# Kernel tuning notes

Measured on AMD Instinct MI355X. Metric: run time of the kernel, lower is better.

## Reference

```python
import jax, jax.numpy as jnp
import numpy as np

B, N, D, K = 16, 1024, 512, 32
EPS = 1e-12  # F.normalize default eps


def setup_inputs() -> dict:
    key = jax.random.key(0)
    k1, k2, k3 = jax.random.split(key, 3)
    x = jax.random.normal(k1, (B, N, D), dtype=jnp.float32)
    mask = (jax.random.uniform(k2, (B, N)) < 0.9).astype(jnp.float32)
    centroids = jax.random.uniform(k3, (D, K), dtype=jnp.float32)
    # _init_params: conv.weight = 2*alpha*centroids, conv.bias = -alpha*||centroids||_col
    W = 2.0 * centroids
    b = -jnp.linalg.norm(centroids, axis=0)
    return {"x": x, "mask": mask, "W": W, "b": b, "centroids": centroids}


def reference(x, mask, W, b, centroids):
    # descriptor-wise L2 normalization (normalize_input=True)
    xn = x / jnp.maximum(jnp.linalg.norm(x, axis=2, keepdims=True), EPS)
    # 1x1 conv (matmul) + bias, masked logits
    logits = (jnp.einsum('bnd,dk->bnk', xn, W) + b) * mask[:, :, None]
    soft_assign = jax.nn.softmax(logits, axis=2) * mask[:, :, None]  # (B,N,K)
    # entropy with -log2(0) -> 0 (matches log_p[isinf]=0 since sa*0 = 0 there)
    safe = jnp.where(soft_assign > 0, soft_assign, 1.0)
    assign_entropy = -(soft_assign * jnp.log2(safe)).sum() / mask.sum()
    # cluster-usage distribution
    assign_sum = soft_assign.sum(axis=1)  # (B,K)
    assign_dist = jax.nn.log_softmax(assign_sum, axis=1)
    # NetVLAD residual pooling, algebraically fused (avoids (B,N,D,K) tensor):
    # vlad[b,d,k] = sum_n xn*sa - centroids[d,k]*sum_n sa
    vlad = jnp.einsum('bnd,bnk->bdk', xn, soft_assign) - centroids[None] * assign_sum[:, None, :]
    vlad = vlad / jnp.maximum(jnp.linalg.norm(vlad, axis=1, keepdims=True), EPS)
    vlad = jnp.transpose(vlad, (0, 2, 1))  # (B,K,D)
    return (vlad, assign_dist, assign_entropy)
```

## Files before the change

### kernel.cpp

```cpp
#include <hip/hip_runtime.h>
#include <math.h>

#define B 16
#define N 1024
#define D 512
#define K 32
#define EPSF 1e-12f

#define WS_WT_F   0
#define WS_CT_F   8192
#define WS_ASP_F  24576
#define WS_ENTP_F 57344
#define WS_MSKP_F 58368
#define WS_PART_F 59392

#define OFF_DIST 262144
#define OFF_ENT  262656

typedef __attribute__((ext_vector_type(8))) short s16x8;
typedef __attribute__((ext_vector_type(4))) short s16x4;
typedef __attribute__((ext_vector_type(4))) float f32x4;

__device__ __forceinline__ ushort f2b(float f) {
    unsigned u = __builtin_bit_cast(unsigned, f);
    u += 0x7fffu + ((u >> 16) & 1u);
    return (ushort)(u >> 16);
}
__device__ __forceinline__ float b2f(ushort u) {
    return __builtin_bit_cast(float, (unsigned)u << 16);
}

__global__ __launch_bounds__(256) void k0_prep(const float* __restrict__ Wf,
    const float* __restrict__ cent, float* __restrict__ ws)
{
    const int t = threadIdx.x;
    const int kk = t >> 3, dseg = (t & 7) * 64;
    if (blockIdx.x == 0) {
        ushort* wt = (ushort*)(ws + WS_WT_F);
        #pragma unroll
        for (int d8 = 0; d8 < 8; ++d8) {
            s16x8 v;
            #pragma unroll
            for (int e = 0; e < 8; ++e)
                v[e] = f2b(Wf[(dseg + d8 * 8 + e) * 32 + kk]);
            *(s16x8*)(wt + kk * 512 + dseg + d8 * 8) = v;
        }
    } else {
        float* ct = ws + WS_CT_F;
        #pragma unroll
        for (int d4 = 0; d4 < 16; ++d4) {
            float4 v;
            v.x = cent[(dseg + d4 * 4 + 0) * 32 + kk];
            v.y = cent[(dseg + d4 * 4 + 1) * 32 + kk];
            v.z = cent[(dseg + d4 * 4 + 2) * 32 + kk];
            v.w = cent[(dseg + d4 * 4 + 3) * 32 + kk];
            *(float4*)(ct + kk * 512 + dseg + d4 * 4) = v;
        }
    }
}

__global__ __launch_bounds__(256, 2) void kA(const float* __restrict__ x,
    const float* __restrict__ mask, const float* __restrict__ bias,
    float* __restrict__ ws, ushort* __restrict__ parts)
{
    __shared__ ushort xs[4 * 2048];
    __shared__ ushort xsT[512 * 36];
    __shared__ ushort tls[32 * 32];
    __shared__ float4 accsh[2 * 128];
    __shared__ float ssqsh[32], invsh[32];

    const int bid = blockIdx.x;
    const int b = bid >> 5;
    const int s = bid & 31;
    const int tid = threadIdx.x;
    const int w = tid >> 6;
    const int rw = w & 1, dw = w >> 1;
    const int l = tid & 63;
    const int g = l >> 4, lo = l & 15;
    const int n0 = s * 32 + rw * 16;
    const int p = bid * 2 + rw;
    const ushort* wt = (const ushort*)(ws + WS_WT_F);

    ushort* xw = xs + w * 2048;
    float ssq[8] = {0.f, 0.f, 0.f, 0.f, 0.f, 0.f, 0.f, 0.f};
    f32x4 acc[2] = {{0.f, 0.f, 0.f, 0.f}, {0.f, 0.f, 0.f, 0.f}};
    const float4* xg = (const float4*)(x + (size_t)(b * N + n0) * D);

    #pragma unroll
    for (int cc = 0; cc < 2; ++cc) {
        const int c = dw * 2 + cc;
        float4 fv[8];
        #pragma unroll
        for (int j = 0; j < 8; ++j) {
            int idx = l + 64 * j;
            fv[j] = xg[(idx >> 5) * 128 + c * 32 + (idx & 31)];
        }
        #pragma unroll
        for (int j = 0; j < 8; ++j)
            ssq[j] += fv[j].x * fv[j].x + fv[j].y * fv[j].y
                    + fv[j].z * fv[j].z + fv[j].w * fv[j].w;
        #pragma unroll
        for (int j = 0; j < 8; ++j) {
            int idx = l + 64 * j;
            int r = idx >> 5, c4 = idx & 31;
            unsigned bo = (unsigned)(c4 * 8) ^ (unsigned)((r & 7) << 4);
            s16x4 sv = { (short)f2b(fv[j].x), (short)f2b(fv[j].y),
                         (short)f2b(fv[j].z), (short)f2b(fv[j].w) };
            *(s16x4*)&xw[r * 128 + (bo >> 1)] = sv;
            int nn = rw * 16 + r;
            int dbase = c * 128 + c4 * 4;
            xsT[(dbase + 0) * 36 + nn] = (ushort)sv[0];
            xsT[(dbase + 1) * 36 + nn] = (ushort)sv[1];
            xsT[(dbase + 2) * 36 + nn] = (ushort)sv[2];
            xsT[(dbase + 3) * 36 + nn] = (ushort)sv[3];
        }
        #pragma unroll
        for (int ks = 0; ks < 4; ++ks) {
            unsigned bo = (unsigned)(ks * 64 + g * 16) ^ (unsigned)((lo & 7) << 4);
            s16x8 bfrag = *(const s16x8*)&xw[lo * 128 + (bo >> 1)];
            int dglob = c * 128 + ks * 32 + g * 8;
            s16x8 a0 = *(const s16x8*)(wt + (size_t)lo * 512 + dglob);
            s16x8 a1 = *(const s16x8*)(wt + (size_t)(16 + lo) * 512 + dglob);
            acc[0] = __builtin_amdgcn_mfma_f32_16x16x32_bf16(a0, bfrag, acc[0], 0, 0, 0);
            acc[1] = __builtin_amdgcn_mfma_f32_16x16x32_bf16(a1, bfrag, acc[1], 0, 0, 0);
        }
    }

    #pragma unroll
    for (int j = 0; j < 8; ++j) {
        #pragma unroll
        for (int m = 16; m; m >>= 1) ssq[j] += __shfl_xor(ssq[j], m);
    }
    if (dw == 1) {
        if ((l & 31) == 0) {
            #pragma unroll
            for (int j = 0; j < 8; ++j)
                ssqsh[rw * 16 + (l >> 5) + 2 * j] = ssq[j];
        }
        accsh[rw * 128 + l * 2 + 0] = *(float4*)&acc[0];
        accsh[rw * 128 + l * 2 + 1] = *(float4*)&acc[1];
    }
    __syncthreads();
    if (dw == 0) {
        float4 o0 = accsh[rw * 128 + l * 2 + 0];
        float4 o1 = accsh[rw * 128 + l * 2 + 1];
        acc[0][0] += o0.x; acc[0][1] += o0.y; acc[0][2] += o0.z; acc[0][3] += o0.w;
        acc[1][0] += o1.x; acc[1][1] += o1.y; acc[1][2] += o1.z; acc[1][3] += o1.w;
        if ((l & 31) == 0) {
            #pragma unroll
            for (int j = 0; j < 8; ++j) {
                int r = (l >> 5) + 2 * j;
                invsh[rw * 16 + r] = 1.f / fmaxf(sqrtf(ssq[j] + ssqsh[rw * 16 + r]), EPSF);
            }
        }
    }
    __syncthreads();
    if (dw == 0) {
        const float inv = invsh[rw * 16 + lo];
        const float mv = mask[b * N + n0 + lo];
        float lg[2][4];
        #pragma unroll
        for (int kt = 0; kt < 2; ++kt)
            #pragma unroll
            for (int r = 0; r < 4; ++r)
                lg[kt][r] = (acc[kt][r] * inv + bias[kt * 16 + g * 4 + r]) * mv;
        float mx = lg[0][0];
        #pragma unroll
        for (int kt = 0; kt < 2; ++kt)
            #pragma unroll
            for (int r = 0; r < 4; ++r) mx = fmaxf(mx, lg[kt][r]);
        mx = fmaxf(mx, __shfl_xor(mx, 16));
        mx = fmaxf(mx, __shfl_xor(mx, 32));
        float e[2][4], sum = 0.f;
        #pragma unroll
        for (int kt = 0; kt < 2; ++kt)
            #pragma unroll
            for (int r = 0; r < 4; ++r) { e[kt][r] = __expf(lg[kt][r] - mx); sum += e[kt][r]; }
        sum += __shfl_xor(sum, 16);
        sum += __shfl_xor(sum, 32);
        const float rs = mv / sum;
        float sa[2][4], ent = 0.f;
        #pragma unroll
        for (int kt = 0; kt < 2; ++kt)
            #pragma unroll
            for (int r = 0; r < 4; ++r) {
                sa[kt][r] = e[kt][r] * rs;
                ent += sa[kt][r] > 0.f ? -sa[kt][r] * __log2f(sa[kt][r]) : 0.f;
            }
        #pragma unroll
        for (int m = 32; m; m >>= 1) ent += __shfl_xor(ent, m);
        if (l == 0) ws[WS_ENTP_F + p] = ent;
        float mp = mv;
        #pragma unroll
        for (int m = 8; m; m >>= 1) mp += __shfl_xor(mp, m);
        if (l == 0) ws[WS_MSKP_F + p] = mp;
        #pragma unroll
        for (int kt = 0; kt < 2; ++kt)
            #pragma unroll
            for (int r = 0; r < 4; ++r) {
                float av = sa[kt][r];
                #pragma unroll
                for (int m = 8; m; m >>= 1) av += __shfl_xor(av, m);
                if (lo == 0) ws[WS_ASP_F + p * 32 + kt * 16 + g * 4 + r] = av;
            }
        #pragma unroll
        for (int kt = 0; kt < 2; ++kt)
            #pragma unroll
            for (int r = 0; r < 4; ++r)
                tls[(kt * 16 + g * 4 + r) * 32 + rw * 16 + lo] = f2b(sa[kt][r] * inv);
    }
    __syncthreads();

    f32x4 acc2[2][8];
    #pragma unroll
    for (int kt = 0; kt < 2; ++kt)
        #pragma unroll
        for (int dt = 0; dt < 8; ++dt)
            acc2[kt][dt] = (f32x4){0.f, 0.f, 0.f, 0.f};
    {
        s16x8 av0 = *(const s16x8*)&tls[lo * 32 + g * 8];
        s16x8 av1 = *(const s16x8*)&tls[(16 + lo) * 32 + g * 8];
        #pragma unroll
        for (int dt = 0; dt < 8; ++dt) {
            int d = w * 128 + dt * 16 + lo;
            s16x4 b0 = *(const s16x4*)&xsT[d * 36 + g * 8];
            s16x4 b1 = *(const s16x4*)&xsT[d * 36 + g * 8 + 4];
            s16x8 bv;
            bv[0] = b0[0]; bv[1] = b0[1]; bv[2] = b0[2]; bv[3] = b0[3];
            bv[4] = b1[0]; bv[5] = b1[1]; bv[6] = b1[2]; bv[7] = b1[3];
            acc2[0][dt] = __builtin_amdgcn_mfma_f32_16x16x32_bf16(av0, bv, acc2[0][dt], 0, 0, 0);
            acc2[1][dt] = __builtin_amdgcn_mfma_f32_16x16x32_bf16(av1, bv, acc2[1][dt], 0, 0, 0);
        }
    }
    __syncthreads();
    ushort* stg = xsT;
    #pragma unroll
    for (int kt = 0; kt < 2; ++kt)
        #pragma unroll
        for (int dt = 0; dt < 8; ++dt)
            #pragma unroll
            for (int r = 0; r < 4; ++r)
                stg[(kt * 16 + g * 4 + r) * 520 + w * 128 + dt * 16 + lo] = f2b(acc2[kt][dt][r]);
    __syncthreads();
    #pragma unroll
    for (int j = 0; j < 8; ++j) {
        int k = w * 8 + j;
        s16x8 v = *(const s16x8*)&stg[k * 520 + l * 8];
        *(s16x8*)(parts + ((size_t)(s * 16 + b) * 32 + k) * 512 + l * 8) = v;
    }
}

__global__ __launch_bounds__(128) void kC(const float* __restrict__ ws,
    const ushort* __restrict__ parts, float* __restrict__ out)
{
    __shared__ float pm[128];
    __shared__ float asL[32];
    __shared__ float red[2];
    const int bid = blockIdx.x;
    const int b = bid >> 5, k = bid & 31;
    const int t = threadIdx.x;
    {
        int kk = t & 31, i = t >> 5;
        float a = 0.f;
        #pragma unroll
        for (int ii = 0; ii < 16; ++ii)
            a += ws[WS_ASP_F + (size_t)(b * 64 + ii * 4 + i) * 32 + kk];
        pm[t] = a;
    }
    __syncthreads();
    if (t < 32) {
        float a = 0.f;
        #pragma unroll
        for (int i = 0; i < 4; ++i) a += pm[i * 32 + t];
        asL[t] = a;
    }
    __syncthreads();
    if (k == 0 && t < 32) {
        float a = asL[t];
        float mx = a;
        #pragma unroll
        for (int m = 16; m; m >>= 1) mx = fmaxf(mx, __shfl_xor(mx, m));
        float e = __expf(a - mx), ssum = e;
        #pragma unroll
        for (int m = 16; m; m >>= 1) ssum += __shfl_xor(ssum, m);
        out[OFF_DIST + b * 32 + t] = a - mx - logf(ssum);
    }
    if (bid == 0 && (t >> 6) == 1) {
        int l = t & 63;
        float es = 0.f, ms = 0.f;
        for (int i = l; i < 1024; i += 64) {
            es += ws[WS_ENTP_F + i];
            ms += ws[WS_MSKP_F + i];
        }
        #pragma unroll
        for (int m = 32; m; m >>= 1) { es += __shfl_xor(es, m); ms += __shfl_xor(ms, m); }
        if (l == 0) out[OFF_ENT] = es / ms;
    }
    const int d0 = t * 4;
    float a0 = 0.f, a1 = 0.f, a2 = 0.f, a3 = 0.f;
    for (int s = 0; s < 32; ++s) {
        s16x4 v = *(const s16x4*)(parts + ((size_t)(s * 16 + b) * 32 + k) * 512 + d0);
        a0 += b2f((ushort)v[0]);
        a1 += b2f((ushort)v[1]);
        a2 += b2f((ushort)v[2]);
        a3 += b2f((ushort)v[3]);
    }
    const float as = asL[k];
    float4 ct = *(const float4*)(ws + WS_CT_F + k * 512 + d0);
    float v0 = a0 - ct.x * as;
    float v1 = a1 - ct.y * as;
    float v2 = a2 - ct.z * as;
    float v3 = a3 - ct.w * as;
    float sq = v0 * v0 + v1 * v1 + v2 * v2 + v3 * v3;
    #pragma unroll
    for (int m = 32; m; m >>= 1) sq += __shfl_xor(sq, m);
    if ((t & 63) == 0) red[t >> 6] = sq;
    __syncthreads();
    float sc = 1.f / fmaxf(sqrtf(red[0] + red[1]), EPSF);
    float4 o = make_float4(v0 * sc, v1 * sc, v2 * sc, v3 * sc);
    *(float4*)(out + (size_t)(b * 32 + k) * 512 + d0) = o;
}

extern "C" void kernel_launch(void* const* d_in, const int* in_sizes, int n_in,
                              void* d_out, int out_size, void* d_ws, size_t ws_size,
                              hipStream_t stream)
{
    const float* x    = (const float*)d_in[0];
    const float* mask = (const float*)d_in[1];
    const float* W    = (const float*)d_in[2];
    const float* bias = (const float*)d_in[3];
    const float* cent = (const float*)d_in[4];
    float* out = (float*)d_out;
    float* ws  = (float*)d_ws;
    ushort* parts = (ushort*)(ws + WS_PART_F);

    k0_prep<<<dim3(2), dim3(256), 0, stream>>>(W, cent, ws);
    kA<<<dim3(512), dim3(256), 0, stream>>>(x, mask, bias, ws, parts);
    kC<<<dim3(512), dim3(128), 0, stream>>>(ws, parts, out);
}
```

Measured before the change: 36.04 us.

## Fuse weight prep into main kernel and process two token tiles per block

Removes the separate prep kernel. Each block of the main kernel now converts W to bf16 into a swizzled LDS buffer, keeps the A fragments in registers, and scatters the centroid transpose into the workspace. Each block handles 64 tokens in two tiles, so the grid drops to 256 blocks and the partial-sum buffer halves. The reduce kernel uses 256 threads and sums 16 partials instead of 32. The trade-off is that every block redoes the W conversion, register pressure rises, and fewer blocks are in flight.

```diff
diff --git a/kernel.cpp b/kernel.cpp
--- a/kernel.cpp
+++ b/kernel.cpp
@@ -7,12 +7,11 @@
 #define K 32
 #define EPSF 1e-12f
 
-#define WS_WT_F   0
-#define WS_CT_F   8192
-#define WS_ASP_F  24576
-#define WS_ENTP_F 57344
-#define WS_MSKP_F 58368
-#define WS_PART_F 59392
+#define WS_CT_F   0
+#define WS_ASP_F  16384
+#define WS_ENTP_F 49152
+#define WS_MSKP_F 50176
+#define WS_PART_F 51200
 
 #define OFF_DIST 262144
 #define OFF_ENT  262656
@@ -30,186 +29,68 @@
     return __builtin_bit_cast(float, (unsigned)u << 16);
 }
 
-__global__ __launch_bounds__(256) void k0_prep(const float* __restrict__ Wf,
-    const float* __restrict__ cent, float* __restrict__ ws)
-{
-    const int t = threadIdx.x;
-    const int kk = t >> 3, dseg = (t & 7) * 64;
-    if (blockIdx.x == 0) {
-        ushort* wt = (ushort*)(ws + WS_WT_F);
-        #pragma unroll
-        for (int d8 = 0; d8 < 8; ++d8) {
-            s16x8 v;
-            #pragma unroll
-            for (int e = 0; e < 8; ++e)
-                v[e] = f2b(Wf[(dseg + d8 * 8 + e) * 32 + kk]);
-            *(s16x8*)(wt + kk * 512 + dseg + d8 * 8) = v;
-        }
-    } else {
-        float* ct = ws + WS_CT_F;
-        #pragma unroll
-        for (int d4 = 0; d4 < 16; ++d4) {
-            float4 v;
-            v.x = cent[(dseg + d4 * 4 + 0) * 32 + kk];
-            v.y = cent[(dseg + d4 * 4 + 1) * 32 + kk];
-            v.z = cent[(dseg + d4 * 4 + 2) * 32 + kk];
-            v.w = cent[(dseg + d4 * 4 + 3) * 32 + kk];
-            *(float4*)(ct + kk * 512 + dseg + d4 * 4) = v;
-        }
-    }
-}
-
-__global__ __launch_bounds__(256, 2) void kA(const float* __restrict__ x,
-    const float* __restrict__ mask, const float* __restrict__ bias,
+struct SH {
+    union U {
+        ushort wtl[32 * 512];
+        struct Q {
+            ushort xs[4 * 2048];
+            ushort xsT[512 * 36];
+        } q;
+    } u;
+    ushort tls[32 * 32];
+    float4 accsh[2 * 128];
+    float ssqsh[32], invsh[32];
+};
+
+__global__ __launch_bounds__(256, 2) void kA2(const float* __restrict__ x,
+    const float* __restrict__ mask, const float* __restrict__ Wf,
+    const float* __restrict__ bias, const float* __restrict__ cent,
     float* __restrict__ ws, ushort* __restrict__ parts)
 {
-    __shared__ ushort xs[4 * 2048];
-    __shared__ ushort xsT[512 * 36];
-    __shared__ ushort tls[32 * 32];
-    __shared__ float4 accsh[2 * 128];
-    __shared__ float ssqsh[32], invsh[32];
-
+    __shared__ SH sh;
     const int bid = blockIdx.x;
-    const int b = bid >> 5;
-    const int s = bid & 31;
+    const int b = bid >> 4;
+    const int s64 = bid & 15;
     const int tid = threadIdx.x;
     const int w = tid >> 6;
     const int rw = w & 1, dw = w >> 1;
     const int l = tid & 63;
     const int g = l >> 4, lo = l & 15;
-    const int n0 = s * 32 + rw * 16;
-    const int p = bid * 2 + rw;
-    const ushort* wt = (const ushort*)(ws + WS_WT_F);
-
-    ushort* xw = xs + w * 2048;
-    float ssq[8] = {0.f, 0.f, 0.f, 0.f, 0.f, 0.f, 0.f, 0.f};
-    f32x4 acc[2] = {{0.f, 0.f, 0.f, 0.f}, {0.f, 0.f, 0.f, 0.f}};
-    const float4* xg = (const float4*)(x + (size_t)(b * N + n0) * D);
-
-    #pragma unroll
-    for (int cc = 0; cc < 2; ++cc) {
-        const int c = dw * 2 + cc;
-        float4 fv[8];
-        #pragma unroll
-        for (int j = 0; j < 8; ++j) {
-            int idx = l + 64 * j;
-            fv[j] = xg[(idx >> 5) * 128 + c * 32 + (idx & 31)];
-        }
-        #pragma unroll
-        for (int j = 0; j < 8; ++j)
-            ssq[j] += fv[j].x * fv[j].x + fv[j].y * fv[j].y
-                    + fv[j].z * fv[j].z + fv[j].w * fv[j].w;
-        #pragma unroll
-        for (int j = 0; j < 8; ++j) {
-            int idx = l + 64 * j;
-            int r = idx >> 5, c4 = idx & 31;
-            unsigned bo = (unsigned)(c4 * 8) ^ (unsigned)((r & 7) << 4);
-            s16x4 sv = { (short)f2b(fv[j].x), (short)f2b(fv[j].y),
-                         (short)f2b(fv[j].z), (short)f2b(fv[j].w) };
-            *(s16x4*)&xw[r * 128 + (bo >> 1)] = sv;
-            int nn = rw * 16 + r;
-            int dbase = c * 128 + c4 * 4;
-            xsT[(dbase + 0) * 36 + nn] = (ushort)sv[0];
-            xsT[(dbase + 1) * 36 + nn] = (ushort)sv[1];
-            xsT[(dbase + 2) * 36 + nn] = (ushort)sv[2];
-            xsT[(dbase + 3) * 36 + nn] = (ushort)sv[3];
-        }
+
+    if (tid < 64) {
+        int k = tid & 31, dd = tid >> 5;
+        int d = bid * 2 + dd;
+        ws[WS_CT_F + k * 512 + d] = cent[d * 32 + k];
+    }
+    {
+        const float4* Wg = (const float4*)Wf;
+        #pragma unroll
+        for (int i = 0; i < 16; ++i) {
+            int f4 = tid + i * 256;
+            float4 v = Wg[f4];
+            int d = f4 >> 3, k4 = (f4 & 7) << 2;
+            float vv[4] = {v.x, v.y, v.z, v.w};
+            #pragma unroll
+            for (int j = 0; j < 4; ++j) {
+                int k = k4 + j;
+                sh.u.wtl[(k * 512 + d) ^ ((k & 7) << 3)] = f2b(vv[j]);
+            }
+        }
+    }
+    __syncthreads();
+    s16x8 afr0[2][4], afr1[2][4];
+    #pragma unroll
+    for (int cc = 0; cc < 2; ++cc)
         #pragma unroll
         for (int ks = 0; ks < 4; ++ks) {
-            unsigned bo = (unsigned)(ks * 64 + g * 16) ^ (unsigned)((lo & 7) << 4);
-            s16x8 bfrag = *(const s16x8*)&xw[lo * 128 + (bo >> 1)];
-            int dglob = c * 128 + ks * 32 + g * 8;
-            s16x8 a0 = *(const s16x8*)(wt + (size_t)lo * 512 + dglob);
-            s16x8 a1 = *(const s16x8*)(wt + (size_t)(16 + lo) * 512 + dglob);
-            acc[0] = __builtin_amdgcn_mfma_f32_16x16x32_bf16(a0, bfrag, acc[0], 0, 0, 0);
-            acc[1] = __builtin_amdgcn_mfma_f32_16x16x32_bf16(a1, bfrag, acc[1], 0, 0, 0);
-        }
-    }
-
-    #pragma unroll
-    for (int j = 0; j < 8; ++j) {
-        #pragma unroll
-        for (int m = 16; m; m >>= 1) ssq[j] += __shfl_xor(ssq[j], m);
-    }
-    if (dw == 1) {
-        if ((l & 31) == 0) {
-            #pragma unroll
-            for (int j = 0; j < 8; ++j)
-                ssqsh[rw * 16 + (l >> 5) + 2 * j] = ssq[j];
-        }
-        accsh[rw * 128 + l * 2 + 0] = *(float4*)&acc[0];
-        accsh[rw * 128 + l * 2 + 1] = *(float4*)&acc[1];
-    }
-    __syncthreads();
-    if (dw == 0) {
-        float4 o0 = accsh[rw * 128 + l * 2 + 0];
-        float4 o1 = accsh[rw * 128 + l * 2 + 1];
-        acc[0][0] += o0.x; acc[0][1] += o0.y; acc[0][2] += o0.z; acc[0][3] += o0.w;
-        acc[1][0] += o1.x; acc[1][1] += o1.y; acc[1][2] += o1.z; acc[1][3] += o1.w;
-        if ((l & 31) == 0) {
-            #pragma unroll
-            for (int j = 0; j < 8; ++j) {
-                int r = (l >> 5) + 2 * j;
-                invsh[rw * 16 + r] = 1.f / fmaxf(sqrtf(ssq[j] + ssqsh[rw * 16 + r]), EPSF);
-            }
-        }
-    }
-    __syncthreads();
-    if (dw == 0) {
-        const float inv = invsh[rw * 16 + lo];
-        const float mv = mask[b * N + n0 + lo];
-        float lg[2][4];
-        #pragma unroll
-        for (int kt = 0; kt < 2; ++kt)
-            #pragma unroll
-            for (int r = 0; r < 4; ++r)
-                lg[kt][r] = (acc[kt][r] * inv + bias[kt * 16 + g * 4 + r]) * mv;
-        float mx = lg[0][0];
-        #pragma unroll
-        for (int kt = 0; kt < 2; ++kt)
-            #pragma unroll
-            for (int r = 0; r < 4; ++r) mx = fmaxf(mx, lg[kt][r]);
-        mx = fmaxf(mx, __shfl_xor(mx, 16));
-        mx = fmaxf(mx, __shfl_xor(mx, 32));
-        float e[2][4], sum = 0.f;
-        #pragma unroll
-        for (int kt = 0; kt < 2; ++kt)
-            #pragma unroll
-            for (int r = 0; r < 4; ++r) { e[kt][r] = __expf(lg[kt][r] - mx); sum += e[kt][r]; }
-        sum += __shfl_xor(sum, 16);
-        sum += __shfl_xor(sum, 32);
-        const float rs = mv / sum;
-        float sa[2][4], ent = 0.f;
-        #pragma unroll
-        for (int kt = 0; kt < 2; ++kt)
-            #pragma unroll
-            for (int r = 0; r < 4; ++r) {
-                sa[kt][r] = e[kt][r] * rs;
-                ent += sa[kt][r] > 0.f ? -sa[kt][r] * __log2f(sa[kt][r]) : 0.f;
-            }
-        #pragma unroll
-        for (int m = 32; m; m >>= 1) ent += __shfl_xor(ent, m);
-        if (l == 0) ws[WS_ENTP_F + p] = ent;
-        float mp = mv;
-        #pragma unroll
-        for (int m = 8; m; m >>= 1) mp += __shfl_xor(mp, m);
-        if (l == 0) ws[WS_MSKP_F + p] = mp;
-        #pragma unroll
-        for (int kt = 0; kt < 2; ++kt)
-            #pragma unroll
-            for (int r = 0; r < 4; ++r) {
-                float av = sa[kt][r];
-                #pragma unroll
-                for (int m = 8; m; m >>= 1) av += __shfl_xor(av, m);
-                if (lo == 0) ws[WS_ASP_F + p * 32 + kt * 16 + g * 4 + r] = av;
-            }
-        #pragma unroll
-        for (int kt = 0; kt < 2; ++kt)
-            #pragma unroll
-            for (int r = 0; r < 4; ++r)
-                tls[(kt * 16 + g * 4 + r) * 32 + rw * 16 + lo] = f2b(sa[kt][r] * inv);
-    }
-    __syncthreads();
+            int dglob = (dw * 2 + cc) * 128 + ks * 32 + g * 8;
+            afr0[cc][ks] = *(const s16x8*)&sh.u.wtl[(lo * 512 + dglob) ^ ((lo & 7) << 3)];
+            afr1[cc][ks] = *(const s16x8*)&sh.u.wtl[((16 + lo) * 512 + dglob) ^ ((lo & 7) << 3)];
+        }
+    __syncthreads();
+
+    ushort* xw = sh.u.q.xs + w * 2048;
+    ushort* xsT = sh.u.q.xsT;
 
     f32x4 acc2[2][8];
     #pragma unroll
@@ -217,23 +98,157 @@
         #pragma unroll
         for (int dt = 0; dt < 8; ++dt)
             acc2[kt][dt] = (f32x4){0.f, 0.f, 0.f, 0.f};
-    {
-        s16x8 av0 = *(const s16x8*)&tls[lo * 32 + g * 8];
-        s16x8 av1 = *(const s16x8*)&tls[(16 + lo) * 32 + g * 8];
-        #pragma unroll
-        for (int dt = 0; dt < 8; ++dt) {
-            int d = w * 128 + dt * 16 + lo;
-            s16x4 b0 = *(const s16x4*)&xsT[d * 36 + g * 8];
-            s16x4 b1 = *(const s16x4*)&xsT[d * 36 + g * 8 + 4];
-            s16x8 bv;
-            bv[0] = b0[0]; bv[1] = b0[1]; bv[2] = b0[2]; bv[3] = b0[3];
-            bv[4] = b1[0]; bv[5] = b1[1]; bv[6] = b1[2]; bv[7] = b1[3];
-            acc2[0][dt] = __builtin_amdgcn_mfma_f32_16x16x32_bf16(av0, bv, acc2[0][dt], 0, 0, 0);
-            acc2[1][dt] = __builtin_amdgcn_mfma_f32_16x16x32_bf16(av1, bv, acc2[1][dt], 0, 0, 0);
-        }
-    }
-    __syncthreads();
-    ushort* stg = xsT;
+
+    #pragma unroll
+    for (int tile = 0; tile < 2; ++tile) {
+        const int n0 = s64 * 64 + tile * 32 + rw * 16;
+        const int p = bid * 4 + tile * 2 + rw;
+
+        float ssq[8] = {0.f, 0.f, 0.f, 0.f, 0.f, 0.f, 0.f, 0.f};
+        f32x4 acc[2] = {{0.f, 0.f, 0.f, 0.f}, {0.f, 0.f, 0.f, 0.f}};
+        const float4* xg = (const float4*)(x + (size_t)(b * N + n0) * D);
+
+        #pragma unroll
+        for (int cc = 0; cc < 2; ++cc) {
+            const int c = dw * 2 + cc;
+            float4 fv[8];
+            #pragma unroll
+            for (int j = 0; j < 8; ++j) {
+                int idx = l + 64 * j;
+                fv[j] = xg[(idx >> 5) * 128 + c * 32 + (idx & 31)];
+            }
+            #pragma unroll
+            for (int j = 0; j < 8; ++j)
+                ssq[j] += fv[j].x * fv[j].x + fv[j].y * fv[j].y
+                        + fv[j].z * fv[j].z + fv[j].w * fv[j].w;
+            #pragma unroll
+            for (int j = 0; j < 8; ++j) {
+                int idx = l + 64 * j;
+                int r = idx >> 5, c4 = idx & 31;
+                unsigned bo = (unsigned)(c4 * 8) ^ (unsigned)((r & 7) << 4);
+                s16x4 sv = { (short)f2b(fv[j].x), (short)f2b(fv[j].y),
+                             (short)f2b(fv[j].z), (short)f2b(fv[j].w) };
+                *(s16x4*)&xw[r * 128 + (bo >> 1)] = sv;
+                int nn = rw * 16 + r;
+                int dbase = c * 128 + c4 * 4;
+                xsT[(dbase + 0) * 36 + nn] = (ushort)sv[0];
+                xsT[(dbase + 1) * 36 + nn] = (ushort)sv[1];
+                xsT[(dbase + 2) * 36 + nn] = (ushort)sv[2];
+                xsT[(dbase + 3) * 36 + nn] = (ushort)sv[3];
+            }
+            #pragma unroll
+            for (int ks = 0; ks < 4; ++ks) {
+                unsigned bo = (unsigned)(ks * 64 + g * 16) ^ (unsigned)((lo & 7) << 4);
+                s16x8 bfrag = *(const s16x8*)&xw[lo * 128 + (bo >> 1)];
+                acc[0] = __builtin_amdgcn_mfma_f32_16x16x32_bf16(afr0[cc][ks], bfrag, acc[0], 0, 0, 0);
+                acc[1] = __builtin_amdgcn_mfma_f32_16x16x32_bf16(afr1[cc][ks], bfrag, acc[1], 0, 0, 0);
+            }
+        }
+
+        #pragma unroll
+        for (int j = 0; j < 8; ++j) {
+            #pragma unroll
+            for (int m = 16; m; m >>= 1) ssq[j] += __shfl_xor(ssq[j], m);
+        }
+        if (dw == 1) {
+            if ((l & 31) == 0) {
+                #pragma unroll
+                for (int j = 0; j < 8; ++j)
+                    sh.ssqsh[rw * 16 + (l >> 5) + 2 * j] = ssq[j];
+            }
+            sh.accsh[rw * 128 + l * 2 + 0] = *(float4*)&acc[0];
+            sh.accsh[rw * 128 + l * 2 + 1] = *(float4*)&acc[1];
+        }
+        __syncthreads();
+        if (dw == 0) {
+            float4 o0 = sh.accsh[rw * 128 + l * 2 + 0];
+            float4 o1 = sh.accsh[rw * 128 + l * 2 + 1];
+            acc[0][0] += o0.x; acc[0][1] += o0.y; acc[0][2] += o0.z; acc[0][3] += o0.w;
+            acc[1][0] += o1.x; acc[1][1] += o1.y; acc[1][2] += o1.z; acc[1][3] += o1.w;
+            if ((l & 31) == 0) {
+                #pragma unroll
+                for (int j = 0; j < 8; ++j) {
+                    int r = (l >> 5) + 2 * j;
+                    sh.invsh[rw * 16 + r] = 1.f / fmaxf(sqrtf(ssq[j] + sh.ssqsh[rw * 16 + r]), EPSF);
+                }
+            }
+        }
+        __syncthreads();
+        if (dw == 0) {
+            const float inv = sh.invsh[rw * 16 + lo];
+            const float mv = mask[b * N + n0 + lo];
+            float lg[2][4];
+            #pragma unroll
+            for (int kt = 0; kt < 2; ++kt)
+                #pragma unroll
+                for (int r = 0; r < 4; ++r)
+                    lg[kt][r] = (acc[kt][r] * inv + bias[kt * 16 + g * 4 + r]) * mv;
+            float mx = lg[0][0];
+            #pragma unroll
+            for (int kt = 0; kt < 2; ++kt)
+                #pragma unroll
+                for (int r = 0; r < 4; ++r) mx = fmaxf(mx, lg[kt][r]);
+            mx = fmaxf(mx, __shfl_xor(mx, 16));
+            mx = fmaxf(mx, __shfl_xor(mx, 32));
+            float e[2][4], sum = 0.f;
+            #pragma unroll
+            for (int kt = 0; kt < 2; ++kt)
+                #pragma unroll
+                for (int r = 0; r < 4; ++r) { e[kt][r] = __expf(lg[kt][r] - mx); sum += e[kt][r]; }
+            sum += __shfl_xor(sum, 16);
+            sum += __shfl_xor(sum, 32);
+            const float rs = mv / sum;
+            float sa[2][4], ent = 0.f;
+            #pragma unroll
+            for (int kt = 0; kt < 2; ++kt)
+                #pragma unroll
+                for (int r = 0; r < 4; ++r) {
+                    sa[kt][r] = e[kt][r] * rs;
+                    ent += sa[kt][r] > 0.f ? -sa[kt][r] * __log2f(sa[kt][r]) : 0.f;
+                }
+            #pragma unroll
+            for (int m = 32; m; m >>= 1) ent += __shfl_xor(ent, m);
+            if (l == 0) ws[WS_ENTP_F + p] = ent;
+            float mp = mv;
+            #pragma unroll
+            for (int m = 8; m; m >>= 1) mp += __shfl_xor(mp, m);
+            if (l == 0) ws[WS_MSKP_F + p] = mp;
+            #pragma unroll
+            for (int kt = 0; kt < 2; ++kt)
+                #pragma unroll
+                for (int r = 0; r < 4; ++r) {
+                    float av = sa[kt][r];
+                    #pragma unroll
+                    for (int m = 8; m; m >>= 1) av += __shfl_xor(av, m);
+                    if (lo == 0) ws[WS_ASP_F + p * 32 + kt * 16 + g * 4 + r] = av;
+                }
+            #pragma unroll
+            for (int kt = 0; kt < 2; ++kt)
+                #pragma unroll
+                for (int r = 0; r < 4; ++r)
+                    sh.tls[(kt * 16 + g * 4 + r) * 32 + rw * 16 + lo] = f2b(sa[kt][r] * inv);
+        }
+        __syncthreads();
+
+        {
+            s16x8 av0 = *(const s16x8*)&sh.tls[lo * 32 + g * 8];
+            s16x8 av1 = *(const s16x8*)&sh.tls[(16 + lo) * 32 + g * 8];
+            #pragma unroll
+            for (int dt = 0; dt < 8; ++dt) {
+                int d = w * 128 + dt * 16 + lo;
+                s16x4 b0 = *(const s16x4*)&xsT[d * 36 + g * 8];
+                s16x4 b1 = *(const s16x4*)&xsT[d * 36 + g * 8 + 4];
+                s16x8 bv;
+                bv[0] = b0[0]; bv[1] = b0[1]; bv[2] = b0[2]; bv[3] = b0[3];
+                bv[4] = b1[0]; bv[5] = b1[1]; bv[6] = b1[2]; bv[7] = b1[3];
+                acc2[0][dt] = __builtin_amdgcn_mfma_f32_16x16x32_bf16(av0, bv, acc2[0][dt], 0, 0, 0);
+                acc2[1][dt] = __builtin_amdgcn_mfma_f32_16x16x32_bf16(av1, bv, acc2[1][dt], 0, 0, 0);
+            }
+        }
+        __syncthreads();
+    }
+
+    ushort* stg = sh.u.q.xsT;
     #pragma unroll
     for (int kt = 0; kt < 2; ++kt)
         #pragma unroll
@@ -246,16 +261,16 @@
     for (int j = 0; j < 8; ++j) {
         int k = w * 8 + j;
         s16x8 v = *(const s16x8*)&stg[k * 520 + l * 8];
-        *(s16x8*)(parts + ((size_t)(s * 16 + b) * 32 + k) * 512 + l * 8) = v;
-    }
-}
-
-__global__ __launch_bounds__(128) void kC(const float* __restrict__ ws,
+        *(s16x8*)(parts + ((size_t)(s64 * 16 + b) * 32 + k) * 512 + l * 8) = v;
+    }
+}
+
+__global__ __launch_bounds__(256) void kC2(const float* __restrict__ ws,
     const ushort* __restrict__ parts, float* __restrict__ out)
 {
-    __shared__ float pm[128];
+    __shared__ float pm[256];
     __shared__ float asL[32];
-    __shared__ float red[2];
+    __shared__ float red[4];
     const int bid = blockIdx.x;
     const int b = bid >> 5, k = bid & 31;
     const int t = threadIdx.x;
@@ -263,15 +278,15 @@
         int kk = t & 31, i = t >> 5;
         float a = 0.f;
         #pragma unroll
-        for (int ii = 0; ii < 16; ++ii)
-            a += ws[WS_ASP_F + (size_t)(b * 64 + ii * 4 + i) * 32 + kk];
+        for (int ii = 0; ii < 8; ++ii)
+            a += ws[WS_ASP_F + (size_t)(b * 64 + ii * 8 + i) * 32 + kk];
         pm[t] = a;
     }
     __syncthreads();
     if (t < 32) {
         float a = 0.f;
         #pragma unroll
-        for (int i = 0; i < 4; ++i) a += pm[i * 32 + t];
+        for (int i = 0; i < 8; ++i) a += pm[i * 32 + t];
         asL[t] = a;
     }
     __syncthreads();
@@ -286,39 +301,36 @@
         out[OFF_DIST + b * 32 + t] = a - mx - logf(ssum);
     }
     if (bid == 0 && (t >> 6) == 1) {
-        int l = t & 63;
+        int ll = t & 63;
         float es = 0.f, ms = 0.f;
-        for (int i = l; i < 1024; i += 64) {
+        for (int i = ll; i < 1024; i += 64) {
             es += ws[WS_ENTP_F + i];
             ms += ws[WS_MSKP_F + i];
         }
         #pragma unroll
         for (int m = 32; m; m >>= 1) { es += __shfl_xor(es, m); ms += __shfl_xor(ms, m); }
-        if (l == 0) out[OFF_ENT] = es / ms;
-    }
-    const int d0 = t * 4;
-    float a0 = 0.f, a1 = 0.f, a2 = 0.f, a3 = 0.f;
-    for (int s = 0; s < 32; ++s) {
-        s16x4 v = *(const s16x4*)(parts + ((size_t)(s * 16 + b) * 32 + k) * 512 + d0);
-        a0 += b2f((ushort)v[0]);
-        a1 += b2f((ushort)v[1]);
-        a2 += b2f((ushort)v[2]);
-        a3 += b2f((ushort)v[3]);
+        if (ll == 0) out[OFF_ENT] = es / ms;
     }
     const float as = asL[k];
-    float4 ct = *(const float4*)(ws + WS_CT_F + k * 512 + d0);
-    float v0 = a0 - ct.x * as;
-    float v1 = a1 - ct.y * as;
-    float v2 = a2 - ct.z * as;
-    float v3 = a3 - ct.w * as;
-    float sq = v0 * v0 + v1 * v1 + v2 * v2 + v3 * v3;
+    const int d0 = t * 2;
+    float a0 = 0.f, a1 = 0.f;
+    #pragma unroll
+    for (int s = 0; s < 16; ++s) {
+        unsigned v = *(const unsigned*)(parts + ((size_t)(s * 16 + b) * 32 + k) * 512 + d0);
+        a0 += b2f((ushort)(v & 0xffffu));
+        a1 += b2f((ushort)(v >> 16));
+    }
+    float2 ctv = *(const float2*)(ws + WS_CT_F + (size_t)k * 512 + d0);
+    float v0 = a0 - ctv.x * as;
+    float v1 = a1 - ctv.y * as;
+    float sq = v0 * v0 + v1 * v1;
     #pragma unroll
     for (int m = 32; m; m >>= 1) sq += __shfl_xor(sq, m);
     if ((t & 63) == 0) red[t >> 6] = sq;
     __syncthreads();
-    float sc = 1.f / fmaxf(sqrtf(red[0] + red[1]), EPSF);
-    float4 o = make_float4(v0 * sc, v1 * sc, v2 * sc, v3 * sc);
-    *(float4*)(out + (size_t)(b * 32 + k) * 512 + d0) = o;
+    float sc = 1.f / fmaxf(sqrtf(red[0] + red[1] + red[2] + red[3]), EPSF);
+    float2 o = make_float2(v0 * sc, v1 * sc);
+    *(float2*)(out + (size_t)(b * 32 + k) * 512 + d0) = o;
 }
 
 extern "C" void kernel_launch(void* const* d_in, const int* in_sizes, int n_in,
@@ -334,7 +346,6 @@
     float* ws  = (float*)d_ws;
     ushort* parts = (ushort*)(ws + WS_PART_F);
 
-    k0_prep<<<dim3(2), dim3(256), 0, stream>>>(W, cent, ws);
-    kA<<<dim3(512), dim3(256), 0, stream>>>(x, mask, bias, ws, parts);
-    kC<<<dim3(512), dim3(128), 0, stream>>>(ws, parts, out);
-}
+    kA2<<<dim3(256), dim3(256), 0, stream>>>(x, mask, W, bias, cent, ws, parts);
+    kC2<<<dim3(512), dim3(256), 0, stream>>>(ws, parts, out);
+}
```

Result: faster. 30.15 us (-16.3%).
